# Kernel tuning notes

Measured on AMD Instinct MI355X. Metric: run time of the kernel, lower is better.

Reference implementation:

```python
import jax, jax.numpy as jnp
import numpy as np

B, S, E, H = 4, 2048, 1024, 16
HD = E // H  # head_dim = 64


def setup_inputs() -> dict:
    key = jax.random.key(0)
    k1, k2, k3, k4 = jax.random.split(key, 4)
    x = jax.random.normal(k1, (B, S, E), dtype=jnp.float32)
    Wqkv = jax.random.normal(k2, (3 * E, E), dtype=jnp.float32) * (E ** -0.5)
    Wo = jax.random.normal(k3, (E, E), dtype=jnp.float32) * (E ** -0.5)
    bo = jax.random.normal(k4, (E,), dtype=jnp.float32) * 0.01
    return {"x": x, "Wqkv": Wqkv, "Wo": Wo, "bo": bo}


def reference(x, Wqkv, Wo, bo):
    b, s, e = x.shape
    # qkv projection (nn.Linear without bias: x @ W^T) -> (b, s, 3e)
    qkv = x @ Wqkv.T
    # reshape (b, s, H, 3*HD) -> (b, H, s, 3*HD), then chunk into q,k,v
    qkv = qkv.reshape(b, s, H, 3 * HD).transpose(0, 2, 1, 3)
    q, k, v = jnp.split(qkv, 3, axis=-1)  # each (b, H, s, HD)
    scale = 1.0 / jnp.sqrt(jnp.asarray(HD, dtype=x.dtype))
    scores = jnp.einsum('bhqd,bhkd->bhqk', q, k) * scale  # (b, H, s, s)
    causal = jnp.tril(jnp.ones((s, s), dtype=bool))
    scores = jnp.where(causal, scores, -jnp.inf)
    probs = jax.nn.softmax(scores, axis=-1)
    out = jnp.einsum('bhqk,bhkd->bhqd', probs, v)  # (b, H, s, HD)
    out = out.transpose(0, 2, 1, 3).reshape(b, s, e)
    return out @ Wo.T + bo
```

## Files before the change

### kernel.cpp

```cpp
#include <hip/hip_runtime.h>
#include <stdint.h>

#define Bn 4
#define Sn 2048
#define En 1024
#define Hn 16
#define HDn 64

typedef __bf16 bf16;
typedef __bf16 bf16x4 __attribute__((ext_vector_type(4)));
typedef __bf16 bf16x8 __attribute__((ext_vector_type(8)));
typedef float  f32x4  __attribute__((ext_vector_type(4)));
typedef float  f32x16 __attribute__((ext_vector_type(16)));
typedef uint32_t u32x4 __attribute__((ext_vector_type(4)));

#define GLDS(gp, lp) __builtin_amdgcn_global_load_lds( \
    (const __attribute__((address_space(1))) void*)(gp), \
    (__attribute__((address_space(3))) void*)(lp), 16, 0, 0)

__global__ __launch_bounds__(256) void cvt_f32_to_bf16(
    const float* __restrict__ in, bf16* __restrict__ out, int n4)
{
    int i = blockIdx.x * 256 + threadIdx.x;
    if (i >= n4) return;
    float4 f = reinterpret_cast<const float4*>(in)[i];
    bf16x4 o;
    o[0] = (bf16)f.x; o[1] = (bf16)f.y; o[2] = (bf16)f.z; o[3] = (bf16)f.w;
    reinterpret_cast<bf16x4*>(out)[i] = o;
}

template<int MODE>
__global__ __launch_bounds__(256) void gemm_bt(
    const bf16* __restrict__ A, const bf16* __restrict__ Bw,
    int M, int N, int K,
    bf16* __restrict__ q_out, bf16* __restrict__ k_out, bf16* __restrict__ v_out,
    float* __restrict__ c_out, const float* __restrict__ bias)
{
    __shared__ bf16 lA[128*64];
    __shared__ bf16 lB[128*64];
    const int tid  = threadIdx.x;
    const int lane = tid & 63;
    const int wv   = tid >> 6;
    const int wm = wv >> 1, wn = wv & 1;
    const int m0 = blockIdx.y * 128;
    const int n0 = blockIdx.x * 128;
    const int lr = lane & 15, lg = lane >> 4;

    f32x4 acc[4][4] = {};

    const int rowA = wv*8 + (lane>>3);
    const int col8 = (lane&7)*8;

    for (int k0 = 0; k0 < K; k0 += 64) {
        #pragma unroll
        for (int c = 0; c < 4; ++c) {
            int row = c*32 + rowA;
            GLDS(A  + (size_t)(m0+row)*K + k0 + col8, lA + (c*32 + wv*8)*64);
            GLDS(Bw + (size_t)(n0+row)*K + k0 + col8, lB + (c*32 + wv*8)*64);
        }
        __syncthreads();
        #pragma unroll
        for (int kk = 0; kk < 64; kk += 32) {
            bf16x8 af[4], bfv[4];
            #pragma unroll
            for (int i = 0; i < 4; ++i)
                af[i] = *reinterpret_cast<const bf16x8*>(lA + (wm*64 + i*16 + lr)*64 + kk + lg*8);
            #pragma unroll
            for (int j = 0; j < 4; ++j)
                bfv[j] = *reinterpret_cast<const bf16x8*>(lB + (wn*64 + j*16 + lr)*64 + kk + lg*8);
            #pragma unroll
            for (int i = 0; i < 4; ++i)
                #pragma unroll
                for (int j = 0; j < 4; ++j)
                    acc[i][j] = __builtin_amdgcn_mfma_f32_16x16x32_bf16(af[i], bfv[j], acc[i][j], 0, 0, 0);
        }
        __syncthreads();
    }

    #pragma unroll
    for (int i = 0; i < 4; ++i) {
        #pragma unroll
        for (int j = 0; j < 4; ++j) {
            const int colb = n0 + wn*64 + j*16 + lr;
            #pragma unroll
            for (int r = 0; r < 4; ++r) {
                const int rowb = m0 + wm*64 + i*16 + lg*4 + r;
                const float v = acc[i][j][r];
                if (MODE == 0) {
                    const int b = rowb >> 11, s = rowb & (Sn-1);
                    const int h = colb / 192, rr = colb - h*192;
                    const int wq = rr >> 6, hd = rr & 63;
                    const size_t off = (((size_t)(b*Hn + h))*Sn + s)*HDn + hd;
                    const bf16 bv = (bf16)v;
                    if (wq == 0)      q_out[off] = bv;
                    else if (wq == 1) k_out[off] = bv;
                    else              v_out[off] = bv;
                } else {
                    c_out[(size_t)rowb*N + colb] = v + bias[colb];
                }
            }
        }
    }
}

static __device__ __forceinline__ uint32_t pkbf(float lo, float hi)
{
    uint16_t a = __builtin_bit_cast(uint16_t, (bf16)lo);
    uint16_t b = __builtin_bit_cast(uint16_t, (bf16)hi);
    return (uint32_t)a | ((uint32_t)b << 16);
}

__global__ __launch_bounds__(512) void attn_fwd(
    const bf16* __restrict__ Q, const bf16* __restrict__ Kg, const bf16* __restrict__ Vg,
    bf16* __restrict__ O)
{
    __shared__ __align__(16) bf16 Kl[64*64];
    __shared__ __align__(16) bf16 Vt[64*64];

    const int tid  = threadIdx.x;
    const int lane = tid & 63;
    const int w    = tid >> 6;
    const int col  = lane & 31;
    const int hv   = lane >> 5;
    const int bh   = blockIdx.x;
    const int qb   = (gridDim.y - 1) - blockIdx.y;
    const int q0w  = qb*256 + w*32;
    const int qg   = q0w + col;

    const bf16* Qb = Q  + (size_t)bh*Sn*HDn;
    const bf16* Kb = Kg + (size_t)bh*Sn*HDn;
    const bf16* Vb = Vg + (size_t)bh*Sn*HDn;

    bf16x8 aq[4];
    #pragma unroll
    for (int ks = 0; ks < 4; ++ks)
        aq[ks] = *reinterpret_cast<const bf16x8*>(Qb + (size_t)qg*HDn + ks*16 + hv*8);

    f32x16 ov[2] = {};
    float m_run = -1e30f, l_run = 0.f;

    const int srow = tid >> 3;
    const int scol = tid & 7;
    const int ksw  = scol ^ (srow & 7);

    const int nkt = 4*(qb+1);
    for (int kt = 0; kt < nkt; ++kt) {
        const int k0 = kt*64;
        __syncthreads();
        GLDS(Kb + (size_t)(k0 + srow)*HDn + ksw*8, Kl + (size_t)w*512);
        {
            bf16x8 vv = *reinterpret_cast<const bf16x8*>(Vb + (size_t)(k0 + srow)*HDn + scol*8);
            #pragma unroll
            for (int j = 0; j < 8; ++j) {
                const int chunk = (scol*8 + j)*8 + ((srow>>3) ^ scol);
                Vt[chunk*8 + (srow&7)] = vv[j];
            }
        }
        __syncthreads();

        if (k0 > q0w + 31) continue;

        f32x16 st[2] = {};
        #pragma unroll
        for (int kb = 0; kb < 2; ++kb) {
            const int key = kb*32 + col;
            #pragma unroll
            for (int ks = 0; ks < 4; ++ks) {
                const int chunk = key*8 + ((ks*2 + hv) ^ (key & 7));
                bf16x8 kf = *reinterpret_cast<const bf16x8*>(Kl + chunk*8);
                st[kb] = __builtin_amdgcn_mfma_f32_32x32x16_bf16(kf, aq[ks], st[kb], 0, 0, 0);
            }
        }

        #pragma unroll
        for (int kb = 0; kb < 2; ++kb)
            #pragma unroll
            for (int r = 0; r < 16; ++r)
                st[kb][r] = st[kb][r] * 0.125f;

        if (k0 + 63 > q0w) {
            #pragma unroll
            for (int kb = 0; kb < 2; ++kb)
                #pragma unroll
                for (int r = 0; r < 16; ++r) {
                    const int keyg = k0 + kb*32 + (r&3) + 8*(r>>2) + 4*hv;
                    if (keyg > qg) st[kb][r] = -1e30f;
                }
        }

        float mx = st[0][0];
        #pragma unroll
        for (int kb = 0; kb < 2; ++kb)
            #pragma unroll
            for (int r = 0; r < 16; ++r)
                mx = fmaxf(mx, st[kb][r]);
        mx = fmaxf(mx, __shfl_xor(mx, 32));
        const float mn = fmaxf(m_run, mx);
        const float fr = __expf(m_run - mn);
        m_run = mn;

        uint32_t wpk[2][8];
        float sum = 0.f;
        #pragma unroll
        for (int kb = 0; kb < 2; ++kb)
            #pragma unroll
            for (int i = 0; i < 8; ++i) {
                const float e0 = __expf(st[kb][2*i]   - mn);
                const float e1 = __expf(st[kb][2*i+1] - mn);
                sum += e0 + e1;
                wpk[kb][i] = pkbf(e0, e1);
            }
        l_run = l_run*fr + sum;
        #pragma unroll
        for (int hb = 0; hb < 2; ++hb)
            #pragma unroll
            for (int r = 0; r < 16; ++r)
                ov[hb][r] *= fr;

        #pragma unroll
        for (int s = 0; s < 4; ++s) {
            const int kb = s >> 1, ls = s & 1;
            const uint32_t send0 = hv ? wpk[kb][4*ls+0] : wpk[kb][4*ls+2];
            const uint32_t send1 = hv ? wpk[kb][4*ls+1] : wpk[kb][4*ls+3];
            const uint32_t keep0 = hv ? wpk[kb][4*ls+2] : wpk[kb][4*ls+0];
            const uint32_t keep1 = hv ? wpk[kb][4*ls+3] : wpk[kb][4*ls+1];
            const uint32_t r0 = (uint32_t)__shfl_xor((int)send0, 32);
            const uint32_t r1 = (uint32_t)__shfl_xor((int)send1, 32);
            u32x4 pwv = { hv ? r0 : keep0, hv ? r1 : keep1,
                          hv ? keep0 : r0, hv ? keep1 : r1 };
            bf16x8 pB = __builtin_bit_cast(bf16x8, pwv);
            #pragma unroll
            for (int hb = 0; hb < 2; ++hb) {
                const int hd = hb*32 + col;
                const int chunk = hd*8 + ((s*2 + hv) ^ ((hd>>3) & 7));
                bf16x8 vf = *reinterpret_cast<const bf16x8*>(Vt + chunk*8);
                ov[hb] = __builtin_amdgcn_mfma_f32_32x32x16_bf16(vf, pB, ov[hb], 0, 0, 0);
            }
        }
    }

    const float lt  = l_run + __shfl_xor(l_run, 32);
    const float inv = 1.0f / lt;
    const int b = bh >> 4, hh = bh & 15;
    bf16* Ob = O + ((size_t)(b*Sn + qg))*En + hh*HDn;
    #pragma unroll
    for (int hb = 0; hb < 2; ++hb)
        #pragma unroll
        for (int g = 0; g < 4; ++g) {
            bf16x4 o4;
            #pragma unroll
            for (int r4 = 0; r4 < 4; ++r4)
                o4[r4] = (bf16)(ov[hb][g*4 + r4] * inv);
            *reinterpret_cast<bf16x4*>(Ob + hb*32 + g*8 + 4*hv) = o4;
        }
}

extern "C" void kernel_launch(void* const* d_in, const int* in_sizes, int n_in,
                              void* d_out, int out_size, void* d_ws, size_t ws_size,
                              hipStream_t stream)
{
    (void)in_sizes; (void)n_in; (void)out_size; (void)ws_size;
    const float* x    = (const float*)d_in[0];
    const float* Wqkv = (const float*)d_in[1];
    const float* Wo   = (const float*)d_in[2];
    const float* bo   = (const float*)d_in[3];
    float* out = (float*)d_out;

    const size_t nBS = (size_t)Bn*Sn;
    char* ws = (char*)d_ws;
    bf16* xb    = (bf16*)ws; ws += nBS*En*2;
    bf16* wqkvb = (bf16*)ws; ws += (size_t)3*En*En*2;
    bf16* wob   = (bf16*)ws; ws += (size_t)En*En*2;
    bf16* Qb    = (bf16*)ws; ws += nBS*En*2;
    bf16* Kb    = (bf16*)ws; ws += nBS*En*2;
    bf16* Vb    = (bf16*)ws; ws += nBS*En*2;
    bf16* AO    = (bf16*)ws; ws += nBS*En*2;

    int n4 = (int)(nBS*En/4);
    cvt_f32_to_bf16<<<(n4+255)/256, 256, 0, stream>>>(x, xb, n4);
    n4 = 3*En*En/4;
    cvt_f32_to_bf16<<<(n4+255)/256, 256, 0, stream>>>(Wqkv, wqkvb, n4);
    n4 = En*En/4;
    cvt_f32_to_bf16<<<(n4+255)/256, 256, 0, stream>>>(Wo, wob, n4);

    gemm_bt<0><<<dim3(3*En/128, nBS/128), 256, 0, stream>>>(
        xb, wqkvb, (int)nBS, 3*En, En, Qb, Kb, Vb, nullptr, nullptr);

    attn_fwd<<<dim3(Bn*Hn, Sn/256), 512, 0, stream>>>(Qb, Kb, Vb, AO);

    gemm_bt<1><<<dim3(En/128, nBS/128), 256, 0, stream>>>(
        AO, wob, (int)nBS, En, En, nullptr, nullptr, nullptr, out, bo);
}
```

Before: 205.5 us.

## Add 256x256 double-buffered QKV GEMM and lazy-rescale exp2 softmax in attention

Replaces the 128x128 QKV projection GEMM with a new 256x256-tile, 512-thread kernel. It double-buffers LDS through global_load_lds, interleaves staging with MFMA sub-blocks under explicit barriers and waitcnts, and raises wave priority around the MFMAs. The aim is more data reuse per tile and overlap of loads with compute. The attention kernel also folds the 1/8 scale and log2e into an exp2 argument via fma, and skips the running-max rescale of the output and sum unless the new max exceeds the old by more than 8 (in log2 units). This cuts per-tile VALU work, but it risks intermediate values up to 2^8 before bf16 packing, and the large-LDS GEMM may limit occupancy.

New measurement: 197.1 us. 4.1% less time.

```diff
diff --git a/kernel.cpp b/kernel.cpp
--- a/kernel.cpp
+++ b/kernel.cpp
@@ -18,6 +18,11 @@
     (const __attribute__((address_space(1))) void*)(gp), \
     (__attribute__((address_space(3))) void*)(lp), 16, 0, 0)
 
+#define BAR() __builtin_amdgcn_s_barrier()
+#define WLG() do { asm volatile("s_waitcnt lgkmcnt(0)" ::: "memory"); \
+                   __builtin_amdgcn_sched_barrier(0); } while (0)
+#define WVM4() asm volatile("s_waitcnt vmcnt(4)" ::: "memory")
+
 __global__ __launch_bounds__(256) void cvt_f32_to_bf16(
     const float* __restrict__ in, bf16* __restrict__ out, int n4)
 {
@@ -27,6 +32,152 @@
     bf16x4 o;
     o[0] = (bf16)f.x; o[1] = (bf16)f.y; o[2] = (bf16)f.z; o[3] = (bf16)f.w;
     reinterpret_cast<bf16x4*>(out)[i] = o;
+}
+
+template<int MODE>
+__global__ __launch_bounds__(512, 2) void gemm256(
+    const bf16* __restrict__ Ag, const bf16* __restrict__ Bw,
+    int M, int N, int K,
+    bf16* __restrict__ q_out, bf16* __restrict__ k_out, bf16* __restrict__ v_out,
+    float* __restrict__ c_out, const float* __restrict__ bias)
+{
+    __shared__ __align__(16) bf16 lA[2 * 256 * 64];
+    __shared__ __align__(16) bf16 lB[2 * 256 * 64];
+
+    const int tid  = threadIdx.x;
+    const int lane = tid & 63;
+    const int w    = tid >> 6;
+    const int wm = w >> 2, wn = w & 3;
+    const int lr = lane & 15, lg = lane >> 4;
+    const int m0 = blockIdx.y * 256;
+    const int n0 = blockIdx.x * 256;
+    const int NT = K >> 6;
+    const int niter = NT >> 1;
+
+    const int srow = tid >> 3;
+    const int sck  = (tid & 7) ^ ((tid >> 3) & 7);
+
+    f32x4 acc[8][4] = {};
+
+    auto stageA = [&](int t, int half) {
+        const int ts = t < NT ? t : NT - 1;
+        bf16* Ld = lA + ((t & 1) ? 16384 : 0) + (half*128 + w*8) * 64;
+        const bf16* S = Ag + (size_t)(m0 + half*128 + srow) * K + ts*64 + sck*8;
+        GLDS(S, Ld);
+        GLDS(S + (size_t)64 * K, Ld + 64 * 64);
+    };
+    auto stageB = [&](int t, int half) {
+        const int ts = t < NT ? t : NT - 1;
+        bf16* Ld = lB + ((t & 1) ? 16384 : 0) + (half*128 + w*8) * 64;
+        const bf16* S = Bw + (size_t)(n0 + half*128 + srow) * K + ts*64 + sck*8;
+        GLDS(S, Ld);
+        GLDS(S + (size_t)64 * K, Ld + 64 * 64);
+    };
+    auto ldA4 = [&](bf16x8 (&a)[4][2], const bf16* Lb, int qm) {
+        #pragma unroll
+        for (int ii = 0; ii < 4; ++ii) {
+            const bf16* p = Lb + (wm*128 + qm*64 + ii*16 + lr) * 64;
+            #pragma unroll
+            for (int kk = 0; kk < 2; ++kk)
+                a[ii][kk] = *reinterpret_cast<const bf16x8*>(p + (((kk << 2) + lg) ^ (lr & 7)) * 8);
+        }
+    };
+    auto ldB2 = [&](bf16x8 (&b)[2][2], const bf16* Lb, int qn) {
+        #pragma unroll
+        for (int j = 0; j < 2; ++j) {
+            const bf16* p = Lb + (wn*64 + qn*32 + j*16 + lr) * 64;
+            #pragma unroll
+            for (int kk = 0; kk < 2; ++kk)
+                b[j][kk] = *reinterpret_cast<const bf16x8*>(p + (((kk << 2) + lg) ^ (lr & 7)) * 8);
+        }
+    };
+    auto mmac = [&](const bf16x8 (&a)[4][2], const bf16x8 (&b)[2][2], int qm, int qn) {
+        __builtin_amdgcn_s_setprio(1);
+        #pragma unroll
+        for (int ii = 0; ii < 4; ++ii)
+            #pragma unroll
+            for (int j = 0; j < 2; ++j)
+                #pragma unroll
+                for (int kk = 0; kk < 2; ++kk)
+                    acc[qm*4 + ii][qn*2 + j] = __builtin_amdgcn_mfma_f32_16x16x32_bf16(
+                        a[ii][kk], b[j][kk], acc[qm*4 + ii][qn*2 + j], 0, 0, 0);
+        __builtin_amdgcn_s_setprio(0);
+    };
+
+    stageA(0, 0); stageA(0, 1); stageB(0, 0); stageB(0, 1);
+    stageB(1, 0); stageB(1, 1);
+    WVM4(); BAR();
+
+    const bf16* A0 = lA;          const bf16* A1 = lA + 16384;
+    const bf16* B0l = lB;         const bf16* B1l = lB + 16384;
+    bf16x8 a[4][2], b0[2][2], b1[2][2];
+
+    for (int i = 0; i < niter; ++i) {
+        const int t = 2 * i;
+        ldA4(a, A0, 0); ldB2(b0, B0l, 0);
+        stageA(t + 1, 0);
+        BAR(); WLG();
+        mmac(a, b0, 0, 0);
+        BAR();
+        ldB2(b1, B0l, 1);
+        stageA(t + 1, 1);
+        BAR(); WLG();
+        mmac(a, b1, 0, 1);
+        BAR();
+        ldA4(a, A0, 1);
+        stageB(t + 2, 0);
+        BAR(); WLG();
+        mmac(a, b0, 1, 0);
+        BAR();
+        stageB(t + 2, 1);
+        WVM4(); BAR();
+        mmac(a, b1, 1, 1);
+        BAR();
+        ldA4(a, A1, 0); ldB2(b0, B1l, 0);
+        stageA(t + 2, 0);
+        BAR(); WLG();
+        mmac(a, b0, 0, 0);
+        BAR();
+        ldB2(b1, B1l, 1);
+        stageA(t + 2, 1);
+        BAR(); WLG();
+        mmac(a, b1, 0, 1);
+        BAR();
+        ldA4(a, A1, 1);
+        stageB(t + 3, 0);
+        BAR(); WLG();
+        mmac(a, b0, 1, 0);
+        BAR();
+        stageB(t + 3, 1);
+        WVM4(); BAR();
+        mmac(a, b1, 1, 1);
+        BAR();
+    }
+
+    #pragma unroll
+    for (int ii = 0; ii < 8; ++ii) {
+        #pragma unroll
+        for (int j = 0; j < 4; ++j) {
+            const int colb = n0 + wn*64 + j*16 + lr;
+            #pragma unroll
+            for (int r = 0; r < 4; ++r) {
+                const int rowb = m0 + wm*128 + ii*16 + lg*4 + r;
+                const float v = acc[ii][j][r];
+                if (MODE == 0) {
+                    const int bb = rowb >> 11, s = rowb & (Sn - 1);
+                    const int h = colb / 192, rr = colb - h*192;
+                    const int wq = rr >> 6, hd = rr & 63;
+                    const size_t off = (((size_t)(bb*Hn + h))*Sn + s)*HDn + hd;
+                    const bf16 bv = (bf16)v;
+                    if (wq == 0)      q_out[off] = bv;
+                    else if (wq == 1) k_out[off] = bv;
+                    else              v_out[off] = bv;
+                } else {
+                    c_out[(size_t)rowb*N + colb] = v + bias[colb];
+                }
+            }
+        }
+    }
 }
 
 template<int MODE>
@@ -137,6 +288,7 @@
         aq[ks] = *reinterpret_cast<const bf16x8*>(Qb + (size_t)qg*HDn + ks*16 + hv*8);
 
     f32x16 ov[2] = {};
+    const float S2 = 0.18033688011112042f;
     float m_run = -1e30f, l_run = 0.f;
 
     const int srow = tid >> 3;
@@ -172,12 +324,6 @@
             }
         }
 
-        #pragma unroll
-        for (int kb = 0; kb < 2; ++kb)
-            #pragma unroll
-            for (int r = 0; r < 16; ++r)
-                st[kb][r] = st[kb][r] * 0.125f;
-
         if (k0 + 63 > q0w) {
             #pragma unroll
             for (int kb = 0; kb < 2; ++kb)
@@ -195,9 +341,19 @@
             for (int r = 0; r < 16; ++r)
                 mx = fmaxf(mx, st[kb][r]);
         mx = fmaxf(mx, __shfl_xor(mx, 32));
-        const float mn = fmaxf(m_run, mx);
-        const float fr = __expf(m_run - mn);
-        m_run = mn;
+        const float smax2 = mx * S2;
+
+        if (!__all(smax2 - m_run <= 8.0f)) {
+            const float mn = fmaxf(m_run, smax2);
+            const float fr = exp2f(m_run - mn);
+            l_run *= fr;
+            #pragma unroll
+            for (int hb = 0; hb < 2; ++hb)
+                #pragma unroll
+                for (int r = 0; r < 16; ++r)
+                    ov[hb][r] *= fr;
+            m_run = mn;
+        }
 
         uint32_t wpk[2][8];
         float sum = 0.f;
@@ -205,17 +361,12 @@
         for (int kb = 0; kb < 2; ++kb)
             #pragma unroll
             for (int i = 0; i < 8; ++i) {
-                const float e0 = __expf(st[kb][2*i]   - mn);
-                const float e1 = __expf(st[kb][2*i+1] - mn);
+                const float e0 = exp2f(fmaf(st[kb][2*i],   S2, -m_run));
+                const float e1 = exp2f(fmaf(st[kb][2*i+1], S2, -m_run));
                 sum += e0 + e1;
                 wpk[kb][i] = pkbf(e0, e1);
             }
-        l_run = l_run*fr + sum;
-        #pragma unroll
-        for (int hb = 0; hb < 2; ++hb)
-            #pragma unroll
-            for (int r = 0; r < 16; ++r)
-                ov[hb][r] *= fr;
+        l_run += sum;
 
         #pragma unroll
         for (int s = 0; s < 4; ++s) {
@@ -283,7 +434,7 @@
     n4 = En*En/4;
     cvt_f32_to_bf16<<<(n4+255)/256, 256, 0, stream>>>(Wo, wob, n4);
 
-    gemm_bt<0><<<dim3(3*En/128, nBS/128), 256, 0, stream>>>(
+    gemm256<0><<<dim3(3*En/256, nBS/256), 512, 0, stream>>>(
         xb, wqkvb, (int)nBS, 3*En, En, Qb, Kb, Vb, nullptr, nullptr);
 
     attn_fwd<<<dim3(Bn*Hn, Sn/256), 512, 0, stream>>>(Qb, Kb, Vb, AO);
```
